# Kernel tuning notes

Hardware: AMD Instinct MI355X
Metric: run time of the kernel (lower is better)

The kernel has to match this reference:

```python
import jax, jax.numpy as jnp
import numpy as np

N = 100000
E = 1600000
IN_DIM = 256
HID = 64


def setup_inputs() -> dict:
    key = jax.random.key(0)
    k1, k2, k3 = jax.random.split(key, 3)
    x = jax.random.normal(k1, (N, IN_DIM), dtype=jnp.float32)
    edge_index = jax.random.randint(k2, (2, E), 0, N, dtype=jnp.int64)
    # glorot-ish init for GCNConv weight, zero bias (PyG default)
    W = jax.random.normal(k3, (IN_DIM, HID), dtype=jnp.float32) * (1.0 / np.sqrt(IN_DIM))
    b = jnp.zeros((HID,), dtype=jnp.float32)
    return {"x": x, "edge_index": edge_index, "W": W, "b": b}


def reference(x, edge_index, W, b):
    # GCNConv: out = D^{-1/2} (A + I) D^{-1/2} (X W) + b
    n = x.shape[0]
    # add self-loops
    loop = jnp.arange(n, dtype=edge_index.dtype)
    src = jnp.concatenate([edge_index[0], loop])  # [E+N]
    dst = jnp.concatenate([edge_index[1], loop])  # [E+N]
    # degree of target nodes (incl. self-loops)
    deg = jax.ops.segment_sum(jnp.ones_like(dst, dtype=x.dtype), dst, num_segments=n)
    dinv = jnp.where(deg > 0, jax.lax.rsqrt(deg), 0.0)  # deg^{-1/2}, inf->0
    norm = dinv[src] * dinv[dst]  # [E+N]
    h = x @ W  # [N, HID] transform before aggregation
    msg = h[src] * norm[:, None]  # gather + scale, [E+N, HID]
    out = jax.ops.segment_sum(msg, dst, num_segments=n)  # scatter-add
    return out + b
```

## Files before the change

### kernel.cpp

```cpp
#include <hip/hip_runtime.h>

typedef float floatx4 __attribute__((ext_vector_type(4)));
typedef short s16x8 __attribute__((ext_vector_type(8)));

#define WG 256
#define NBUCK 512
#define BSH 8
#define EBLK 512
#define CAP 8192
#define MAXIT 16

__device__ inline unsigned pack_bf16_rne(float a, float b) {
    unsigned ua = __float_as_uint(a), ub = __float_as_uint(b);
    ua = (ua + 0x7FFFu + ((ua >> 16) & 1u)) >> 16;
    ub = (ub + 0x7FFFu + ((ub >> 16) & 1u)) >> 16;
    return ua | (ub << 16);
}

union FragU {
    unsigned u[4];
    uint4 q;
    s16x8 v;
};

__global__ __launch_bounds__(WG) void k_packw(const float* __restrict__ W,
                                              uint4* __restrict__ wpack,
                                              int* __restrict__ cursor) {
    const int q = blockIdx.x * WG + threadIdx.x;
    if (q < NBUCK) cursor[q] = 0;
    const int kb = q >> 8, nt = (q >> 6) & 3, ln = q & 63;
    const int quad = ln >> 4, l15 = ln & 15;
    const int col = nt * 16 + l15;
    const int krow = kb * 32 + quad * 8;
    unsigned up[4];
#pragma unroll
    for (int p = 0; p < 4; p++) {
        float a = W[(krow + 2 * p) * 64 + col];
        float b2 = W[(krow + 2 * p + 1) * 64 + col];
        up[p] = pack_bf16_rne(a, b2);
    }
    uint4 pk = {up[0], up[1], up[2], up[3]};
    wpack[q] = pk;
}

__global__ __launch_bounds__(WG, 4) void k_main(const void* __restrict__ ei, int* __restrict__ cursor,
                                                unsigned* __restrict__ ebuf, int E,
                                                const float* __restrict__ x, const uint4* __restrict__ wpack,
                                                unsigned short* __restrict__ g, int N) {
    __shared__ int hh[NBUCK];
    __shared__ int hbase[NBUCK];
    __shared__ int s32flag;
    const int t = threadIdx.x;

    if ((int)blockIdx.x < EBLK) {
        if (t == 0) s32flag = 0;
        for (int i = t; i < NBUCK; i += WG) hh[i] = 0;
        __syncthreads();
        {
            const int* w = (const int*)ei;
            int nz = 0;
            for (int j = t; j < 4096; j += WG) nz |= (w[2 * j + 1] != 0);
            if (nz) atomicOr(&s32flag, 1);
        }
        __syncthreads();
        const bool i32 = (s32flag != 0);
        const int chunk = (E + EBLK - 1) / EBLK;
        const int s = blockIdx.x * chunk;
        const int eend = min(E, s + chunk);

        if (chunk <= MAXIT * WG) {
            unsigned ew[MAXIT];
            unsigned short ebk[MAXIT];
#pragma unroll
            for (int i = 0; i < MAXIT; i++) {
                const int e = s + t + i * WG;
                ebk[i] = 0xFFFFu;
                if (e < eend) {
                    int sN, dN;
                    if (i32) {
                        const int* p = (const int*)ei;
                        sN = p[e];
                        dN = p[E + e];
                    } else {
                        const long long* p = (const long long*)ei;
                        sN = (int)p[e];
                        dN = (int)p[(long long)E + e];
                    }
                    ew[i] = (unsigned)sN | ((unsigned)(dN & 255) << 24);
                    ebk[i] = (unsigned short)(dN >> BSH);
                    atomicAdd(&hh[dN >> BSH], 1);
                }
            }
            __syncthreads();
            for (int i = t; i < NBUCK; i += WG) {
                int c = hh[i];
                hbase[i] = c ? atomicAdd(&cursor[i], c) : 0;
                hh[i] = 0;
            }
            __syncthreads();
#pragma unroll
            for (int i = 0; i < MAXIT; i++) {
                if (ebk[i] != 0xFFFFu) {
                    const int bkt = ebk[i];
                    const int pos = hbase[bkt] + atomicAdd(&hh[bkt], 1);
                    if (pos < CAP) ebuf[(size_t)bkt * CAP + pos] = ew[i];
                }
            }
        } else {
            if (i32) {
                const int* pd = (const int*)ei + E;
                for (int e = s + t; e < eend; e += WG) atomicAdd(&hh[pd[e] >> BSH], 1);
            } else {
                const long long* pd = (const long long*)ei + E;
                for (int e = s + t; e < eend; e += WG) atomicAdd(&hh[(int)pd[e] >> BSH], 1);
            }
            __syncthreads();
            for (int i = t; i < NBUCK; i += WG) {
                int c = hh[i];
                hbase[i] = c ? atomicAdd(&cursor[i], c) : 0;
                hh[i] = 0;
            }
            __syncthreads();
            for (int e = s + t; e < eend; e += WG) {
                int sN, dN;
                if (i32) {
                    const int* p = (const int*)ei;
                    sN = p[e];
                    dN = p[E + e];
                } else {
                    const long long* p = (const long long*)ei;
                    sN = (int)p[e];
                    dN = (int)p[(long long)E + e];
                }
                int bkt = dN >> BSH;
                int pos = hbase[bkt] + atomicAdd(&hh[bkt], 1);
                if (pos < CAP) ebuf[(size_t)bkt * CAP + pos] = (unsigned)sN | ((unsigned)(dN & 255) << 24);
            }
        }
    } else {
        const int bb = blockIdx.x - EBLK;
        const int wv = t >> 6;
        const int lane = t & 63;
        const int quad = lane >> 4, l15 = lane & 15;

        long long arow = (long long)bb * 64 + wv * 16 + l15;
        if (arow >= N) arow = N - 1;
        const float* xr = x + arow * 256 + quad * 8;
        const uint4* wp = wpack + lane;

        floatx4 xv[8][2];
#pragma unroll
        for (int kb = 0; kb < 8; kb++) {
            xv[kb][0] = *(const floatx4*)(xr + kb * 32);
            xv[kb][1] = *(const floatx4*)(xr + kb * 32 + 4);
        }
#pragma unroll
        for (int kb = 0; kb < 8; kb++) {
            asm volatile("" : "+v"(xv[kb][0]), "+v"(xv[kb][1]));
        }
        __builtin_amdgcn_sched_barrier(0);

        floatx4 acc[4];
#pragma unroll
        for (int nt = 0; nt < 4; nt++) acc[nt] = 0.f;

        FragU bc0, bc1, bc2, bc3;
        bc0.q = wp[0 * 64];
        bc1.q = wp[1 * 64];
        bc2.q = wp[2 * 64];
        bc3.q = wp[3 * 64];

#pragma unroll
        for (int kb = 0; kb < 8; kb++) {
            FragU bn0, bn1, bn2, bn3;
            if (kb < 7) {
                bn0.q = wp[((kb + 1) * 4 + 0) * 64];
                bn1.q = wp[((kb + 1) * 4 + 1) * 64];
                bn2.q = wp[((kb + 1) * 4 + 2) * 64];
                bn3.q = wp[((kb + 1) * 4 + 3) * 64];
            }
            FragU a;
            a.u[0] = pack_bf16_rne(xv[kb][0][0], xv[kb][0][1]);
            a.u[1] = pack_bf16_rne(xv[kb][0][2], xv[kb][0][3]);
            a.u[2] = pack_bf16_rne(xv[kb][1][0], xv[kb][1][1]);
            a.u[3] = pack_bf16_rne(xv[kb][1][2], xv[kb][1][3]);
            acc[0] = __builtin_amdgcn_mfma_f32_16x16x32_bf16(a.v, bc0.v, acc[0], 0, 0, 0);
            acc[1] = __builtin_amdgcn_mfma_f32_16x16x32_bf16(a.v, bc1.v, acc[1], 0, 0, 0);
            acc[2] = __builtin_amdgcn_mfma_f32_16x16x32_bf16(a.v, bc2.v, acc[2], 0, 0, 0);
            acc[3] = __builtin_amdgcn_mfma_f32_16x16x32_bf16(a.v, bc3.v, acc[3], 0, 0, 0);
            if (kb < 7) {
                bc0 = bn0;
                bc1 = bn1;
                bc2 = bn2;
                bc3 = bn3;
            }
        }

        const long long orow0 = (long long)bb * 64 + wv * 16 + quad * 4;
#pragma unroll
        for (int r = 0; r < 4; r++) {
            const long long orow = orow0 + r;
            if (orow < N) {
#pragma unroll
                for (int nt = 0; nt < 4; nt++) {
                    float v = acc[nt][r];
                    unsigned uv = __float_as_uint(v);
                    uv = (uv + 0x7FFFu + ((uv >> 16) & 1u)) >> 16;
                    g[orow * 64 + nt * 16 + l15] = (unsigned short)uv;
                }
            }
        }
    }
}

__global__ __launch_bounds__(WG) void k_csr(const unsigned* __restrict__ ebuf, const int* __restrict__ cursor,
                                            int* __restrict__ off, int* __restrict__ srcs,
                                            float* __restrict__ dinv, int N, int nbuse) {
    __shared__ int red[256];
    __shared__ int h[256];
    __shared__ int sc[256];
    __shared__ int cur[256];
    const int t = threadIdx.x;
    const int b = blockIdx.x;
    const int node0 = b << BSH;
    const int rows = min(256, N - node0);
    int part = 0;
    for (int i = t; i < b; i += WG) part += min(cursor[i], CAP);
    red[t] = part;
    h[t] = 0;
    __syncthreads();
    for (int d = WG / 2; d > 0; d >>= 1) {
        if (t < d) red[t] += red[t + d];
        __syncthreads();
    }
    const int ebase = red[0];
    const int cnt = min(cursor[b], CAP);
    const unsigned* eb = ebuf + (size_t)b * CAP;
    for (int j = t; j < cnt; j += WG) atomicAdd(&h[eb[j] >> 24], 1);
    __syncthreads();
    const int deg = (t < rows) ? h[t] + 1 : 0;
    sc[t] = deg;
    __syncthreads();
    for (int d = 1; d < 256; d <<= 1) {
        int a = (t >= d) ? sc[t - d] : 0;
        __syncthreads();
        sc[t] += a;
        __syncthreads();
    }
    const int basef = ebase + node0;
    const int local = sc[t] - deg;
    if (t < rows) {
        off[node0 + t] = basef + local;
        srcs[basef + local] = node0 + t;
        cur[t] = local + 1;
        dinv[node0 + t] = rsqrtf((float)deg);
    }
    if (b == nbuse - 1 && t == 0) off[N] = ebase + cnt + N;
    __syncthreads();
    for (int j = t; j < cnt; j += WG) {
        unsigned w = eb[j];
        int dl = (int)(w >> 24);
        int pos = basef + atomicAdd(&cur[dl], 1);
        srcs[pos] = (int)(w & 0xFFFFFFu);
    }
}

__global__ __launch_bounds__(WG) void k_gather(const unsigned short* __restrict__ g,
                                               const int* __restrict__ off, const int* __restrict__ srcs,
                                               const float* __restrict__ dinv, const float* __restrict__ bias,
                                               float* __restrict__ out, int N) {
    const int t = threadIdx.x;
    const int node = blockIdx.x * 16 + (t >> 4);
    if (node >= N) return;
    const int sub = (t >> 3) & 1;
    const int c8 = (t & 7) * 8;
    const int e0 = off[node], e1 = off[node + 1];
    float a0 = 0.f, a1 = 0.f, a2 = 0.f, a3 = 0.f, a4 = 0.f, a5 = 0.f, a6 = 0.f, a7 = 0.f;

    int e = e0 + sub;
    if (e < e1) {
        int s_cur = srcs[e];
        int en = e + 2;
        int s_nxt = (en < e1) ? srcs[en] : 0;
        float ds = dinv[s_cur];
        uint4 v = *(const uint4*)(g + (long long)s_cur * 64 + c8);
        for (;;) {
            const bool more = en < e1;
            float dsn = 0.f;
            uint4 vn = v;
            int s2 = 0;
            if (more) {
                dsn = dinv[s_nxt];
                vn = *(const uint4*)(g + (long long)s_nxt * 64 + c8);
            }
            const int en2 = en + 2;
            if (en2 < e1) s2 = srcs[en2];
            a0 += ds * __uint_as_float(v.x << 16);
            a1 += ds * __uint_as_float(v.x & 0xFFFF0000u);
            a2 += ds * __uint_as_float(v.y << 16);
            a3 += ds * __uint_as_float(v.y & 0xFFFF0000u);
            a4 += ds * __uint_as_float(v.z << 16);
            a5 += ds * __uint_as_float(v.z & 0xFFFF0000u);
            a6 += ds * __uint_as_float(v.w << 16);
            a7 += ds * __uint_as_float(v.w & 0xFFFF0000u);
            if (!more) break;
            ds = dsn;
            v = vn;
            s_nxt = s2;
            en = en2;
        }
    }

    a0 += __shfl_xor(a0, 8, 64);
    a1 += __shfl_xor(a1, 8, 64);
    a2 += __shfl_xor(a2, 8, 64);
    a3 += __shfl_xor(a3, 8, 64);
    a4 += __shfl_xor(a4, 8, 64);
    a5 += __shfl_xor(a5, 8, 64);
    a6 += __shfl_xor(a6, 8, 64);
    a7 += __shfl_xor(a7, 8, 64);

    if (sub == 0) {
        const float d = dinv[node];
        const floatx4 b0 = *(const floatx4*)(bias + c8);
        const floatx4 b1 = *(const floatx4*)(bias + c8 + 4);
        floatx4 o0, o1;
        o0[0] = d * a0 + b0[0];
        o0[1] = d * a1 + b0[1];
        o0[2] = d * a2 + b0[2];
        o0[3] = d * a3 + b0[3];
        o1[0] = d * a4 + b1[0];
        o1[1] = d * a5 + b1[1];
        o1[2] = d * a6 + b1[2];
        o1[3] = d * a7 + b1[3];
        *(floatx4*)(out + (long long)node * 64 + c8) = o0;
        *(floatx4*)(out + (long long)node * 64 + c8 + 4) = o1;
    }
}

extern "C" void kernel_launch(void* const* d_in, const int* in_sizes, int n_in,
                              void* d_out, int out_size, void* d_ws, size_t ws_size,
                              hipStream_t stream) {
    const float* x = (const float*)d_in[0];
    const void* ei = d_in[1];
    const float* W = (const float*)d_in[2];
    const float* b = (const float*)d_in[3];
    float* out = (float*)d_out;

    const int N = in_sizes[0] / 256;
    const int E = in_sizes[1] / 2;
    const int NBUSE = (N + 255) >> BSH;
    const int GEMMB = (N + 63) / 64;

    char* ws = (char*)d_ws;
    size_t o = 0;
    auto alloc = [&](size_t bytes) -> void* {
        void* p = ws + o;
        o += (bytes + 255) & ~(size_t)255;
        return p;
    };
    float* dinv = (float*)alloc((size_t)N * 4);
    unsigned short* g = (unsigned short*)alloc((size_t)N * 64 * 2);
    unsigned* ebuf = (unsigned*)alloc((size_t)NBUCK * CAP * 4);
    int* cursor = (int*)alloc((size_t)NBUCK * 4);
    int* off = (int*)alloc((size_t)(N + 1) * 4);
    int* srcs = (int*)alloc((size_t)(E + N) * 4);
    uint4* wpack = (uint4*)alloc((size_t)2048 * 16);
    if (o > ws_size) return;

    k_packw<<<8, WG, 0, stream>>>(W, wpack, cursor);
    k_main<<<EBLK + GEMMB, WG, 0, stream>>>(ei, cursor, ebuf, E, x, wpack, g, N);
    k_csr<<<NBUSE, WG, 0, stream>>>(ebuf, cursor, off, srcs, dinv, N, NBUSE);
    k_gather<<<(N + 15) / 16, WG, 0, stream>>>(g, off, srcs, dinv, b, out, N);
}
```

Before: 244.5 us.

## Fuse CSR build and gather into per-bucket LDS aggregation kernel

Merges the CSR-construction and gather kernels into one kernel. Each block sorts its bucket's edges by destination in shared memory and then aggregates directly, so the global off/srcs arrays and one kernel launch are no longer needed. Degrees are now counted with global atomics during bucketing, and dinv is recomputed on the fly with rsqrt from those counts. Buckets shrink to 128 nodes and a capacity of 4096 so the edge list fits in shared memory. The costs are many global atomics on deg, far fewer aggregation blocks (about 782 instead of 6250), and a tighter bucket capacity that could overflow on skewed inputs.

```diff
diff --git a/kernel.cpp b/kernel.cpp
--- a/kernel.cpp
+++ b/kernel.cpp
@@ -4,10 +4,10 @@
 typedef short s16x8 __attribute__((ext_vector_type(8)));
 
 #define WG 256
-#define NBUCK 512
-#define BSH 8
+#define NBUCK 1024
+#define BSH 7
 #define EBLK 512
-#define CAP 8192
+#define CAP 4096
 #define MAXIT 16
 
 __device__ inline unsigned pack_bf16_rne(float a, float b) {
@@ -25,26 +25,30 @@
 
 __global__ __launch_bounds__(WG) void k_packw(const float* __restrict__ W,
                                               uint4* __restrict__ wpack,
-                                              int* __restrict__ cursor) {
+                                              int* __restrict__ cursor,
+                                              int* __restrict__ deg, int N) {
     const int q = blockIdx.x * WG + threadIdx.x;
     if (q < NBUCK) cursor[q] = 0;
-    const int kb = q >> 8, nt = (q >> 6) & 3, ln = q & 63;
-    const int quad = ln >> 4, l15 = ln & 15;
-    const int col = nt * 16 + l15;
-    const int krow = kb * 32 + quad * 8;
-    unsigned up[4];
-#pragma unroll
-    for (int p = 0; p < 4; p++) {
-        float a = W[(krow + 2 * p) * 64 + col];
-        float b2 = W[(krow + 2 * p + 1) * 64 + col];
-        up[p] = pack_bf16_rne(a, b2);
-    }
-    uint4 pk = {up[0], up[1], up[2], up[3]};
-    wpack[q] = pk;
+    for (int z = q; z < N; z += 16384) deg[z] = 0;
+    if (q < 2048) {
+        const int kb = q >> 8, nt = (q >> 6) & 3, ln = q & 63;
+        const int quad = ln >> 4, l15 = ln & 15;
+        const int col = nt * 16 + l15;
+        const int krow = kb * 32 + quad * 8;
+        unsigned up[4];
+#pragma unroll
+        for (int p = 0; p < 4; p++) {
+            float a = W[(krow + 2 * p) * 64 + col];
+            float b2 = W[(krow + 2 * p + 1) * 64 + col];
+            up[p] = pack_bf16_rne(a, b2);
+        }
+        uint4 pk = {up[0], up[1], up[2], up[3]};
+        wpack[q] = pk;
+    }
 }
 
 __global__ __launch_bounds__(WG, 4) void k_main(const void* __restrict__ ei, int* __restrict__ cursor,
-                                                unsigned* __restrict__ ebuf, int E,
+                                                unsigned* __restrict__ ebuf, int* __restrict__ deg, int E,
                                                 const float* __restrict__ x, const uint4* __restrict__ wpack,
                                                 unsigned short* __restrict__ g, int N) {
     __shared__ int hh[NBUCK];
@@ -86,9 +90,10 @@
                         sN = (int)p[e];
                         dN = (int)p[(long long)E + e];
                     }
-                    ew[i] = (unsigned)sN | ((unsigned)(dN & 255) << 24);
+                    ew[i] = (unsigned)sN | ((unsigned)(dN & 127) << 24);
                     ebk[i] = (unsigned short)(dN >> BSH);
                     atomicAdd(&hh[dN >> BSH], 1);
+                    atomicAdd(&deg[dN], 1);
                 }
             }
             __syncthreads();
@@ -109,10 +114,18 @@
         } else {
             if (i32) {
                 const int* pd = (const int*)ei + E;
-                for (int e = s + t; e < eend; e += WG) atomicAdd(&hh[pd[e] >> BSH], 1);
+                for (int e = s + t; e < eend; e += WG) {
+                    const int dN = pd[e];
+                    atomicAdd(&hh[dN >> BSH], 1);
+                    atomicAdd(&deg[dN], 1);
+                }
             } else {
                 const long long* pd = (const long long*)ei + E;
-                for (int e = s + t; e < eend; e += WG) atomicAdd(&hh[(int)pd[e] >> BSH], 1);
+                for (int e = s + t; e < eend; e += WG) {
+                    const int dN = (int)pd[e];
+                    atomicAdd(&hh[dN >> BSH], 1);
+                    atomicAdd(&deg[dN], 1);
+                }
             }
             __syncthreads();
             for (int i = t; i < NBUCK; i += WG) {
@@ -134,7 +147,7 @@
                 }
                 int bkt = dN >> BSH;
                 int pos = hbase[bkt] + atomicAdd(&hh[bkt], 1);
-                if (pos < CAP) ebuf[(size_t)bkt * CAP + pos] = (unsigned)sN | ((unsigned)(dN & 255) << 24);
+                if (pos < CAP) ebuf[(size_t)bkt * CAP + pos] = (unsigned)sN | ((unsigned)(dN & 127) << 24);
             }
         }
     } else {
@@ -213,128 +226,132 @@
     }
 }
 
-__global__ __launch_bounds__(WG) void k_csr(const unsigned* __restrict__ ebuf, const int* __restrict__ cursor,
-                                            int* __restrict__ off, int* __restrict__ srcs,
-                                            float* __restrict__ dinv, int N, int nbuse) {
-    __shared__ int red[256];
-    __shared__ int h[256];
-    __shared__ int sc[256];
-    __shared__ int cur[256];
+__global__ __launch_bounds__(WG) void k_agg(const unsigned* __restrict__ ebuf, const int* __restrict__ cursor,
+                                            const int* __restrict__ deg, const unsigned short* __restrict__ g,
+                                            const float* __restrict__ bias, float* __restrict__ out, int N) {
+    __shared__ int slist[CAP];
+    __shared__ int h[128];
+    __shared__ int off[128];
+    __shared__ int cur[128];
+    __shared__ int ldg[128];
     const int t = threadIdx.x;
     const int b = blockIdx.x;
     const int node0 = b << BSH;
-    const int rows = min(256, N - node0);
-    int part = 0;
-    for (int i = t; i < b; i += WG) part += min(cursor[i], CAP);
-    red[t] = part;
-    h[t] = 0;
-    __syncthreads();
-    for (int d = WG / 2; d > 0; d >>= 1) {
-        if (t < d) red[t] += red[t + d];
-        __syncthreads();
-    }
-    const int ebase = red[0];
+
+    if (t < 128) h[t] = 0;
+    __syncthreads();
+
     const int cnt = min(cursor[b], CAP);
     const unsigned* eb = ebuf + (size_t)b * CAP;
-    for (int j = t; j < cnt; j += WG) atomicAdd(&h[eb[j] >> 24], 1);
-    __syncthreads();
-    const int deg = (t < rows) ? h[t] + 1 : 0;
-    sc[t] = deg;
-    __syncthreads();
-    for (int d = 1; d < 256; d <<= 1) {
-        int a = (t >= d) ? sc[t - d] : 0;
+
+    unsigned ew[16];
+#pragma unroll
+    for (int i = 0; i < 16; i++) {
+        const int e = t + i * WG;
+        ew[i] = (e < cnt) ? eb[e] : 0xFFFFFFFFu;
+        if (ew[i] != 0xFFFFFFFFu) atomicAdd(&h[(ew[i] >> 24) & 127], 1);
+    }
+    __syncthreads();
+    if (t < 128) {
+        ldg[t] = h[t];
+        off[t] = h[t];
+        cur[t] = 0;
+    }
+    __syncthreads();
+    for (int d = 1; d < 128; d <<= 1) {
+        int a = 0;
+        if (t < 128 && t >= d) a = off[t - d];
         __syncthreads();
-        sc[t] += a;
+        if (t < 128) off[t] += a;
         __syncthreads();
     }
-    const int basef = ebase + node0;
-    const int local = sc[t] - deg;
-    if (t < rows) {
-        off[node0 + t] = basef + local;
-        srcs[basef + local] = node0 + t;
-        cur[t] = local + 1;
-        dinv[node0 + t] = rsqrtf((float)deg);
-    }
-    if (b == nbuse - 1 && t == 0) off[N] = ebase + cnt + N;
-    __syncthreads();
-    for (int j = t; j < cnt; j += WG) {
-        unsigned w = eb[j];
-        int dl = (int)(w >> 24);
-        int pos = basef + atomicAdd(&cur[dl], 1);
-        srcs[pos] = (int)(w & 0xFFFFFFu);
-    }
-}
-
-__global__ __launch_bounds__(WG) void k_gather(const unsigned short* __restrict__ g,
-                                               const int* __restrict__ off, const int* __restrict__ srcs,
-                                               const float* __restrict__ dinv, const float* __restrict__ bias,
-                                               float* __restrict__ out, int N) {
-    const int t = threadIdx.x;
-    const int node = blockIdx.x * 16 + (t >> 4);
-    if (node >= N) return;
+    if (t < 128) off[t] -= ldg[t];
+    __syncthreads();
+#pragma unroll
+    for (int i = 0; i < 16; i++) {
+        if (ew[i] != 0xFFFFFFFFu) {
+            const int dl = (ew[i] >> 24) & 127;
+            const int pos = off[dl] + atomicAdd(&cur[dl], 1);
+            slist[pos] = (int)(ew[i] & 0xFFFFFFu);
+        }
+    }
+    __syncthreads();
+
+    const int gid = t >> 4;
     const int sub = (t >> 3) & 1;
     const int c8 = (t & 7) * 8;
-    const int e0 = off[node], e1 = off[node + 1];
-    float a0 = 0.f, a1 = 0.f, a2 = 0.f, a3 = 0.f, a4 = 0.f, a5 = 0.f, a6 = 0.f, a7 = 0.f;
-
-    int e = e0 + sub;
-    if (e < e1) {
-        int s_cur = srcs[e];
-        int en = e + 2;
-        int s_nxt = (en < e1) ? srcs[en] : 0;
-        float ds = dinv[s_cur];
-        uint4 v = *(const uint4*)(g + (long long)s_cur * 64 + c8);
-        for (;;) {
-            const bool more = en < e1;
-            float dsn = 0.f;
-            uint4 vn = v;
-            int s2 = 0;
-            if (more) {
-                dsn = dinv[s_nxt];
-                vn = *(const uint4*)(g + (long long)s_nxt * 64 + c8);
-            }
-            const int en2 = en + 2;
-            if (en2 < e1) s2 = srcs[en2];
-            a0 += ds * __uint_as_float(v.x << 16);
-            a1 += ds * __uint_as_float(v.x & 0xFFFF0000u);
-            a2 += ds * __uint_as_float(v.y << 16);
-            a3 += ds * __uint_as_float(v.y & 0xFFFF0000u);
-            a4 += ds * __uint_as_float(v.z << 16);
-            a5 += ds * __uint_as_float(v.z & 0xFFFF0000u);
-            a6 += ds * __uint_as_float(v.w << 16);
-            a7 += ds * __uint_as_float(v.w & 0xFFFF0000u);
-            if (!more) break;
-            ds = dsn;
-            v = vn;
-            s_nxt = s2;
-            en = en2;
-        }
-    }
-
-    a0 += __shfl_xor(a0, 8, 64);
-    a1 += __shfl_xor(a1, 8, 64);
-    a2 += __shfl_xor(a2, 8, 64);
-    a3 += __shfl_xor(a3, 8, 64);
-    a4 += __shfl_xor(a4, 8, 64);
-    a5 += __shfl_xor(a5, 8, 64);
-    a6 += __shfl_xor(a6, 8, 64);
-    a7 += __shfl_xor(a7, 8, 64);
-
-    if (sub == 0) {
-        const float d = dinv[node];
-        const floatx4 b0 = *(const floatx4*)(bias + c8);
-        const floatx4 b1 = *(const floatx4*)(bias + c8 + 4);
-        floatx4 o0, o1;
-        o0[0] = d * a0 + b0[0];
-        o0[1] = d * a1 + b0[1];
-        o0[2] = d * a2 + b0[2];
-        o0[3] = d * a3 + b0[3];
-        o1[0] = d * a4 + b1[0];
-        o1[1] = d * a5 + b1[1];
-        o1[2] = d * a6 + b1[2];
-        o1[3] = d * a7 + b1[3];
-        *(floatx4*)(out + (long long)node * 64 + c8) = o0;
-        *(floatx4*)(out + (long long)node * 64 + c8 + 4) = o1;
+    for (int nn = gid; nn < 128; nn += 16) {
+        const int node = node0 + nn;
+        if (node >= N) continue;
+        const int e0 = off[nn], ne = ldg[nn];
+        float a0 = 0.f, a1 = 0.f, a2 = 0.f, a3 = 0.f, a4 = 0.f, a5 = 0.f, a6 = 0.f, a7 = 0.f;
+        int j = sub;
+        if (j < ne) {
+            int s_cur = slist[e0 + j];
+            int jn = j + 2;
+            int s_nxt = (jn < ne) ? slist[e0 + jn] : 0;
+            int dgc = deg[s_cur];
+            uint4 v = *(const uint4*)(g + (size_t)s_cur * 64 + c8);
+            for (;;) {
+                const bool more = jn < ne;
+                int dgn = 0;
+                uint4 vn = v;
+                int s2 = 0;
+                if (more) {
+                    dgn = deg[s_nxt];
+                    vn = *(const uint4*)(g + (size_t)s_nxt * 64 + c8);
+                }
+                const int jn2 = jn + 2;
+                if (jn2 < ne) s2 = slist[e0 + jn2];
+                const float ds = rsqrtf((float)(dgc + 1));
+                a0 += ds * __uint_as_float(v.x << 16);
+                a1 += ds * __uint_as_float(v.x & 0xFFFF0000u);
+                a2 += ds * __uint_as_float(v.y << 16);
+                a3 += ds * __uint_as_float(v.y & 0xFFFF0000u);
+                a4 += ds * __uint_as_float(v.z << 16);
+                a5 += ds * __uint_as_float(v.z & 0xFFFF0000u);
+                a6 += ds * __uint_as_float(v.w << 16);
+                a7 += ds * __uint_as_float(v.w & 0xFFFF0000u);
+                if (!more) break;
+                dgc = dgn;
+                v = vn;
+                s_nxt = s2;
+                jn = jn2;
+            }
+        }
+        a0 += __shfl_xor(a0, 8, 64);
+        a1 += __shfl_xor(a1, 8, 64);
+        a2 += __shfl_xor(a2, 8, 64);
+        a3 += __shfl_xor(a3, 8, 64);
+        a4 += __shfl_xor(a4, 8, 64);
+        a5 += __shfl_xor(a5, 8, 64);
+        a6 += __shfl_xor(a6, 8, 64);
+        a7 += __shfl_xor(a7, 8, 64);
+        if (sub == 0) {
+            const float d = rsqrtf((float)(ldg[nn] + 1));
+            const uint4 vs = *(const uint4*)(g + (size_t)node * 64 + c8);
+            a0 += d * __uint_as_float(vs.x << 16);
+            a1 += d * __uint_as_float(vs.x & 0xFFFF0000u);
+            a2 += d * __uint_as_float(vs.y << 16);
+            a3 += d * __uint_as_float(vs.y & 0xFFFF0000u);
+            a4 += d * __uint_as_float(vs.z << 16);
+            a5 += d * __uint_as_float(vs.z & 0xFFFF0000u);
+            a6 += d * __uint_as_float(vs.w << 16);
+            a7 += d * __uint_as_float(vs.w & 0xFFFF0000u);
+            const floatx4 b0 = *(const floatx4*)(bias + c8);
+            const floatx4 b1 = *(const floatx4*)(bias + c8 + 4);
+            floatx4 o0, o1;
+            o0[0] = d * a0 + b0[0];
+            o0[1] = d * a1 + b0[1];
+            o0[2] = d * a2 + b0[2];
+            o0[3] = d * a3 + b0[3];
+            o1[0] = d * a4 + b1[0];
+            o1[1] = d * a5 + b1[1];
+            o1[2] = d * a6 + b1[2];
+            o1[3] = d * a7 + b1[3];
+            *(floatx4*)(out + (size_t)node * 64 + c8) = o0;
+            *(floatx4*)(out + (size_t)node * 64 + c8 + 4) = o1;
+        }
     }
 }
 
@@ -349,7 +366,7 @@
 
     const int N = in_sizes[0] / 256;
     const int E = in_sizes[1] / 2;
-    const int NBUSE = (N + 255) >> BSH;
+    const int NBUSE = (N + 127) >> BSH;
     const int GEMMB = (N + 63) / 64;
 
     char* ws = (char*)d_ws;
@@ -359,17 +376,14 @@
         o += (bytes + 255) & ~(size_t)255;
         return p;
     };
-    float* dinv = (float*)alloc((size_t)N * 4);
     unsigned short* g = (unsigned short*)alloc((size_t)N * 64 * 2);
     unsigned* ebuf = (unsigned*)alloc((size_t)NBUCK * CAP * 4);
     int* cursor = (int*)alloc((size_t)NBUCK * 4);
-    int* off = (int*)alloc((size_t)(N + 1) * 4);
-    int* srcs = (int*)alloc((size_t)(E + N) * 4);
+    int* deg = (int*)alloc((size_t)N * 4);
     uint4* wpack = (uint4*)alloc((size_t)2048 * 16);
     if (o > ws_size) return;
 
-    k_packw<<<8, WG, 0, stream>>>(W, wpack, cursor);
-    k_main<<<EBLK + GEMMB, WG, 0, stream>>>(ei, cursor, ebuf, E, x, wpack, g, N);
-    k_csr<<<NBUSE, WG, 0, stream>>>(ebuf, cursor, off, srcs, dinv, N, NBUSE);
-    k_gather<<<(N + 15) / 16, WG, 0, stream>>>(g, off, srcs, dinv, b, out, N);
-}
+    k_packw<<<64, WG, 0, stream>>>(W, wpack, cursor, deg, N);
+    k_main<<<EBLK + GEMMB, WG, 0, stream>>>(ei, cursor, ebuf, deg, E, x, wpack, g, N);
+    k_agg<<<NBUSE, WG, 0, stream>>>(ebuf, cursor, deg, g, b, out, N);
+}
```

After: 290.0 us. 18.6% more time.
